# Kernel optimization log

Hardware: AMD Instinct MI355X
Metric: run time of the kernel (lower is better)

The kernel has to match this reference:

```python
import jax, jax.numpy as jnp
import numpy as np

UNITS, ORDER, THETA = 1024, 512, 784.0
T, B = 784, 128

def _lmu_AB(order, theta):
    # Legendre delay continuous-time state space, then ZOH discretization (dt=1)
    q = np.arange(order, dtype=np.float64)
    r = (2.0 * q + 1.0)[:, None] / theta
    i, j = np.meshgrid(q, q, indexing='ij')
    A = np.where(i < j, -1.0, (-1.0) ** (i - j + 1.0)) * r
    Bc = ((-1.0) ** q)[:, None] * r
    Ad = np.array(jax.scipy.linalg.expm(jnp.asarray(A, dtype=jnp.float32)), dtype=np.float64)
    Bd = np.linalg.solve(A, (Ad - np.eye(order)) @ Bc)
    # cell stores AT = Ad - I so that m <- m + m@AT^T + u@BT^T == m@Ad^T + u@Bd^T
    return (Ad - np.eye(order)).astype(np.float32), Bd.astype(np.float32)

def setup_inputs() -> dict:
    key = jax.random.key(0)
    ks = jax.random.split(key, 9)
    AT, BT = _lmu_AB(ORDER, THETA)
    xav = np.sqrt(2.0 / (UNITS + ORDER)).astype(np.float32)
    return {
        'inputs': jax.random.normal(ks[0], (T, B, 1), dtype=jnp.float32),
        'e_x': jax.random.normal(ks[1], (1, 1), dtype=jnp.float32),
        'e_h': jax.random.normal(ks[2], (1, UNITS), dtype=jnp.float32) * 0.02,
        'e_m': jax.random.normal(ks[3], (1, ORDER), dtype=jnp.float32) * 0.02,
        'W_x': jax.random.normal(ks[4], (UNITS, 1), dtype=jnp.float32) * 0.1,
        'W_h': jax.random.normal(ks[5], (UNITS, UNITS), dtype=jnp.float32) * 0.02,
        'W_m': jax.random.normal(ks[6], (UNITS, ORDER), dtype=jnp.float32) * xav,
        'AT': jnp.asarray(AT),
        'BT': jnp.asarray(BT),
        'W_dense': jax.random.normal(ks[7], (10, UNITS), dtype=jnp.float32) * 0.03,
        'b_dense': jax.random.normal(ks[8], (10,), dtype=jnp.float32) * 0.01,
    }

def reference(inputs, e_x, e_h, e_m, W_x, W_h, W_m, AT, BT, W_dense, b_dense):
    Bsz = inputs.shape[1]
    h0 = jnp.zeros((Bsz, W_h.shape[0]), inputs.dtype)
    m0 = jnp.zeros((Bsz, AT.shape[0]), inputs.dtype)
    def step(carry, x):  # x: (B, 1)
        h, m = carry
        u = x @ e_x.T + h @ e_h.T + m @ e_m.T            # (B, 1)
        m = m + m @ AT.T + u @ BT.T                       # linear Legendre memory update
        h = jnp.tanh(x @ W_x.T + h @ W_h.T + m @ W_m.T)  # nonlinear hidden update
        return (h, m), None
    (h, m), _ = jax.lax.scan(step, (h0, m0), inputs)
    logits = h @ W_dense.T + b_dense
    return jax.nn.softmax(logits, axis=-1)
```

## Files before the change

kernel.cpp:

```cpp
#include <hip/hip_runtime.h>
#include <hip/hip_fp16.h>
#include <cmath>


typedef _Float16 half8 __attribute__((ext_vector_type(8)));
typedef float floatx4 __attribute__((ext_vector_type(4)));

#define NSTATE   1536
#define BATCH    128
#define TSTEPS   784
#define KTILES   48
#define ISL_WGS  32
#define SLICE_H8 9216
#define LO_SCALE 2048.0f
#define LO_INV   (1.0f / 2048.0f)

__device__ __align__(16) _Float16 g_Whi[NSTATE * NSTATE];
__device__ __align__(16) _Float16 g_Wlo[NSTATE * NSTATE];
__device__ float    g_wb[NSTATE];
__device__ float    g_WmA[1024 * 512];
__device__ float    g_WmB[1024];
__device__ __align__(16) _Float16 g_Shi[2 * BATCH * NSTATE];
__device__ __align__(16) _Float16 g_Slo[2 * BATCH * NSTATE];
__device__ unsigned g_bar[1024];

__device__ __forceinline__ unsigned poll_rmw(unsigned* p) {
    unsigned old;
    asm volatile("global_atomic_add %0, %1, %2, off sc0\n\ts_waitcnt vmcnt(0)"
                 : "=&v"(old)
                 : "v"(p), "v"(0u)
                 : "memory");
    return old;
}

__device__ __forceinline__ float fast_tanh(float x) {
    float e = __expf(2.f * x);
    return 1.f - 2.f / (e + 1.f);
}

__global__ void prep_wmb(const float* __restrict__ Wm, const float* __restrict__ BT) {
    int row  = blockIdx.x * 4 + (threadIdx.x >> 6);
    int lane = threadIdx.x & 63;
    float s = 0.f;
    for (int c = lane; c < 512; c += 64) s += Wm[row * 512 + c] * BT[c];
    for (int o = 32; o; o >>= 1) s += __shfl_down(s, o);
    if (lane == 0) g_WmB[row] = s;
}

__global__ void prep_wma(const float* __restrict__ Wm, const float* __restrict__ AT) {
    __shared__ float As[32][33], Bs[32][33];
    int d0 = blockIdx.x * 32, i0 = blockIdx.y * 32;
    int tx = threadIdx.x & 31, ty = threadIdx.x >> 5;
    float acc[4];
#pragma unroll
    for (int r = 0; r < 4; ++r) acc[r] = Wm[(i0 + ty + 8 * r) * 512 + d0 + tx];
    for (int c0 = 0; c0 < 512; c0 += 32) {
#pragma unroll
        for (int r = 0; r < 4; ++r) {
            As[ty + 8 * r][tx] = Wm[(i0 + ty + 8 * r) * 512 + c0 + tx];
            Bs[ty + 8 * r][tx] = AT[(c0 + ty + 8 * r) * 512 + d0 + tx];
        }
        __syncthreads();
#pragma unroll
        for (int c = 0; c < 32; ++c)
#pragma unroll
            for (int r = 0; r < 4; ++r) acc[r] += As[ty + 8 * r][c] * Bs[c][tx];
        __syncthreads();
    }
#pragma unroll
    for (int r = 0; r < 4; ++r) g_WmA[(i0 + ty + 8 * r) * 512 + d0 + tx] = acc[r];
}

__global__ void prep_wfull(const float* __restrict__ Wh, const float* __restrict__ AT,
                           const float* __restrict__ BT, const float* __restrict__ eh,
                           const float* __restrict__ em, const float* __restrict__ ex,
                           const float* __restrict__ Wx) {
    int s = blockIdx.x * 256 + threadIdx.x;
    int j8 = s & 7;
    int u = s >> 3;
    int lane = u & 63;
    u >>= 6;
    int nt = u % 3; u /= 3;
    int kt = u % 48;
    int sl = u / 48;
    int n = sl * 48 + nt * 16 + (lane & 15);
    int k = kt * 32 + ((lane >> 4) & 3) * 8 + j8;

    float w;
    if (n < 1024) {
        if (k < 1024) w = Wh[n * 1024 + k] + g_WmB[n] * eh[k];
        else          w = g_WmA[n * 512 + (k - 1024)] + g_WmB[n] * em[k - 1024];
    } else {
        int c = n - 1024;
        if (k < 1024) w = BT[c] * eh[k];
        else {
            int d = k - 1024;
            w = ((c == d) ? 1.f : 0.f) + AT[c * 512 + d] + BT[c] * em[d];
        }
    }
    _Float16 hi = (_Float16)w;
    g_Whi[s] = hi;
    g_Wlo[s] = (_Float16)((w - (float)hi) * LO_SCALE);

    if (s < NSTATE) {
        float b = (s < 1024) ? (Wx[s] + ex[0] * g_WmB[s]) : (BT[s - 1024] * ex[0]);
        g_wb[s] = b;
    }
    if (s < 2 * BATCH * NSTATE) { g_Shi[s] = (_Float16)0.f; g_Slo[s] = (_Float16)0.f; }
    if (s < 1024) g_bar[s] = 0u;
}

__launch_bounds__(256, 1)
__global__ void lmu_persist(const float* __restrict__ inputs) {
    __shared__ half8  lwh[SLICE_H8];
    __shared__ float4 red[4 * 3 * 64];
    __shared__ int    s_sl;

    const int tid = threadIdx.x;

    unsigned xcd;
    asm volatile("s_getreg_b32 %0, hwreg(HW_REG_XCC_ID)" : "=s"(xcd));
    xcd &= 7u;
    if (tid == 0) {
        unsigned rank = __hip_atomic_fetch_add(g_bar + 512 + xcd * 64, 1u,
                                               __ATOMIC_RELAXED,
                                               __HIP_MEMORY_SCOPE_WORKGROUP);
        s_sl = (int)(rank & 31u);
    }
    __syncthreads();
    const int isl = (int)xcd;
    const int sl  = s_sl;

    {
        const half8* src = (const half8*)g_Whi + (size_t)sl * SLICE_H8;
        for (int i = tid; i < SLICE_H8; i += 256) lwh[i] = src[i];
    }

    const int lane = tid & 63, wv = tid >> 6;
    const int quad = lane >> 4, l16 = lane & 15;
    const int kt0 = wv * 12;
    const int rowA = isl * 16 + l16;
    unsigned* cnt = g_bar + isl * 64;

    const int ncol = sl * 48 + wv * 16 + l16;
    const float wbv = (wv < 3) ? g_wb[ncol] : 0.f;
    const bool do_tanh = (sl * 48 + wv * 16) < 1024;

    half8 wr[12 * 3];
    {
        const half8* wlo = (const half8*)g_Wlo + (size_t)sl * SLICE_H8;
#pragma unroll
        for (int ki = 0; ki < 12; ++ki)
#pragma unroll
            for (int nt = 0; nt < 3; ++nt)
                wr[ki * 3 + nt] = wlo[((kt0 + ki) * 3 + nt) * 64 + lane];
    }

    __syncthreads();

    int buf = 0;
    for (int t = 0; t < TSTEPS; ++t) {
        const _Float16* shr =
            g_Shi + buf * BATCH * NSTATE + rowA * NSTATE + quad * 8;
        const _Float16* slr =
            g_Slo + buf * BATCH * NSTATE + rowA * NSTATE + quad * 8;

        floatx4 aA[3], aB[3], aC[3];
#pragma unroll
        for (int q = 0; q < 3; ++q) { aA[q] = (floatx4)0.f; aB[q] = (floatx4)0.f; aC[q] = (floatx4)0.f; }

#pragma unroll
        for (int ki = 0; ki < 12; ++ki) {
            const int kt = kt0 + ki;
            half8 ah = *(const half8*)(shr + kt * 32);
            half8 al = *(const half8*)(slr + kt * 32);
#pragma unroll
            for (int nt = 0; nt < 3; ++nt) {
                half8 bh = lwh[(kt * 3 + nt) * 64 + lane];
                aA[nt] = __builtin_amdgcn_mfma_f32_16x16x32_f16(ah, bh, aA[nt], 0, 0, 0);
                aB[nt] = __builtin_amdgcn_mfma_f32_16x16x32_f16(al, bh, aB[nt], 0, 0, 0);
                aC[nt] = __builtin_amdgcn_mfma_f32_16x16x32_f16(ah, wr[ki * 3 + nt], aC[nt], 0, 0, 0);
            }
        }

#pragma unroll
        for (int nt = 0; nt < 3; ++nt) {
            floatx4 P = aA[nt] + (aB[nt] + aC[nt]) * LO_INV;
            red[(wv * 3 + nt) * 64 + lane] = float4{P[0], P[1], P[2], P[3]};
        }
        __syncthreads();

        const int nbuf = buf ^ 1;
        if (wv < 3) {
            float4 v0 = red[(0 * 3 + wv) * 64 + lane];
            float4 v1 = red[(1 * 3 + wv) * 64 + lane];
            float4 v2 = red[(2 * 3 + wv) * 64 + lane];
            float4 v3 = red[(3 * 3 + wv) * 64 + lane];
            float vr4[4] = {v0.x + v1.x + v2.x + v3.x, v0.y + v1.y + v2.y + v3.y,
                            v0.z + v1.z + v2.z + v3.z, v0.w + v1.w + v2.w + v3.w};
            _Float16* dh = g_Shi + nbuf * BATCH * NSTATE;
            _Float16* dl = g_Slo + nbuf * BATCH * NSTATE;
            const float* xt = inputs + t * BATCH + isl * 16 + quad * 4;
#pragma unroll
            for (int r = 0; r < 4; ++r) {
                int b = isl * 16 + quad * 4 + r;
                float v = vr4[r] + xt[r] * wbv;
                if (do_tanh) v = fast_tanh(v);
                _Float16 hi = (_Float16)v;
                dh[b * NSTATE + ncol] = hi;
                dl[b * NSTATE + ncol] = (_Float16)((v - (float)hi) * LO_SCALE);
            }
        }

        __builtin_amdgcn_fence(__ATOMIC_RELEASE, "workgroup");
        __syncthreads();
        if (tid == 0) {
            __hip_atomic_fetch_add(cnt, 1u, __ATOMIC_RELAXED,
                                   __HIP_MEMORY_SCOPE_WORKGROUP);
            const unsigned target = (unsigned)ISL_WGS * (unsigned)(t + 1);
            int spin = 0;
            while (poll_rmw(cnt) < target) {
                if (++spin > (1 << 18)) break;
            }
        }
        __syncthreads();
        asm volatile("buffer_inv\n\ts_waitcnt vmcnt(0)" ::: "memory");
        __builtin_amdgcn_fence(__ATOMIC_ACQUIRE, "workgroup");
        buf = nbuf;
    }
}

__global__ void lmu_out(const float* __restrict__ Wd, const float* __restrict__ bd,
                        float* __restrict__ out) {
    __shared__ float red[272];
    int b = blockIdx.x;
    const _Float16* sh = g_Shi + b * NSTATE;
    const _Float16* sl = g_Slo + b * NSTATE;
    int tid = threadIdx.x;
    int c = tid & 15, chunk = tid >> 4;
    float part = 0.f;
    if (c < 10) {
        for (int i = chunk * 64; i < chunk * 64 + 64; ++i)
            part += ((float)sh[i] + (float)sl[i] * LO_INV) * Wd[c * 1024 + i];
    }
    red[chunk * 16 + c] = part;
    __syncthreads();
    if (tid < 10) {
        float lg = bd[tid];
        for (int q = 0; q < 16; ++q) lg += red[q * 16 + tid];
        red[256 + tid] = lg;
    }
    __syncthreads();
    if (tid < 10) {
        float mx = red[256];
        for (int q = 1; q < 10; ++q) mx = fmaxf(mx, red[256 + q]);
        float sm = 0.f;
        for (int q = 0; q < 10; ++q) sm += expf(red[256 + q] - mx);
        out[b * 10 + tid] = expf(red[256 + tid] - mx) / sm;
    }
}

extern "C" void kernel_launch(void* const* d_in, const int* in_sizes, int n_in,
                              void* d_out, int out_size, void* d_ws, size_t ws_size,
                              hipStream_t stream) {
    const float* inputs = (const float*)d_in[0];
    const float* e_x    = (const float*)d_in[1];
    const float* e_h    = (const float*)d_in[2];
    const float* e_m    = (const float*)d_in[3];
    const float* W_x    = (const float*)d_in[4];
    const float* W_h    = (const float*)d_in[5];
    const float* W_m    = (const float*)d_in[6];
    const float* AT     = (const float*)d_in[7];
    const float* BT     = (const float*)d_in[8];
    const float* W_d    = (const float*)d_in[9];
    const float* b_d    = (const float*)d_in[10];
    (void)d_ws; (void)ws_size; (void)in_sizes; (void)n_in;

    prep_wmb<<<256, 256, 0, stream>>>(W_m, BT);
    prep_wma<<<dim3(16, 32), 256, 0, stream>>>(W_m, AT);
    prep_wfull<<<9216, 256, 0, stream>>>(W_h, AT, BT, e_h, e_m, e_x, W_x);

    lmu_persist<<<256, 256, 0, stream>>>(inputs);

    lmu_out<<<128, 256, 0, stream>>>(W_d, b_d, (float*)d_out);
}
```

Before: 3.910 ms.

## Split K across eight waves per workgroup with two-stage LDS reduction

The persistent LMU kernel goes from 4 to 8 waves per workgroup, and each wave covers 6 K-tiles instead of 12, so the per-wave MFMA chain and register-resident low-part weights are halved. Partial sums are reduced through LDS in two phases: waves 0-3 store, then waves 4-7 accumulate, with an extra barrier. The aim is to cut per-step latency on the serial recurrence by running more MFMA streams in parallel. The cost is one more __syncthreads per timestep and a launch bound of 2 blocks per CU, which may limit registers.

```diff
diff --git a/kernel.cpp b/kernel.cpp
--- a/kernel.cpp
+++ b/kernel.cpp
@@ -14,6 +14,8 @@
 #define SLICE_H8 9216
 #define LO_SCALE 2048.0f
 #define LO_INV   (1.0f / 2048.0f)
+#define NWAVES   8
+#define KI_W     6
 
 __device__ __align__(16) _Float16 g_Whi[NSTATE * NSTATE];
 __device__ __align__(16) _Float16 g_Wlo[NSTATE * NSTATE];
@@ -110,11 +112,11 @@
     if (s < 1024) g_bar[s] = 0u;
 }
 
-__launch_bounds__(256, 1)
+__launch_bounds__(512, 2)
 __global__ void lmu_persist(const float* __restrict__ inputs) {
-    __shared__ half8  lwh[SLICE_H8];
-    __shared__ float4 red[4 * 3 * 64];
-    __shared__ int    s_sl;
+    __shared__ half8   lwh[SLICE_H8];
+    __shared__ floatx4 red[4 * 3 * 64];
+    __shared__ int     s_sl;
 
     const int tid = threadIdx.x;
 
@@ -133,12 +135,12 @@
 
     {
         const half8* src = (const half8*)g_Whi + (size_t)sl * SLICE_H8;
-        for (int i = tid; i < SLICE_H8; i += 256) lwh[i] = src[i];
+        for (int i = tid; i < SLICE_H8; i += 512) lwh[i] = src[i];
     }
 
     const int lane = tid & 63, wv = tid >> 6;
     const int quad = lane >> 4, l16 = lane & 15;
-    const int kt0 = wv * 12;
+    const int kt0 = wv * KI_W;
     const int rowA = isl * 16 + l16;
     unsigned* cnt = g_bar + isl * 64;
 
@@ -146,11 +148,11 @@
     const float wbv = (wv < 3) ? g_wb[ncol] : 0.f;
     const bool do_tanh = (sl * 48 + wv * 16) < 1024;
 
-    half8 wr[12 * 3];
+    half8 wr[KI_W * 3];
     {
         const half8* wlo = (const half8*)g_Wlo + (size_t)sl * SLICE_H8;
 #pragma unroll
-        for (int ki = 0; ki < 12; ++ki)
+        for (int ki = 0; ki < KI_W; ++ki)
 #pragma unroll
             for (int nt = 0; nt < 3; ++nt)
                 wr[ki * 3 + nt] = wlo[((kt0 + ki) * 3 + nt) * 64 + lane];
@@ -170,7 +172,7 @@
         for (int q = 0; q < 3; ++q) { aA[q] = (floatx4)0.f; aB[q] = (floatx4)0.f; aC[q] = (floatx4)0.f; }
 
 #pragma unroll
-        for (int ki = 0; ki < 12; ++ki) {
+        for (int ki = 0; ki < KI_W; ++ki) {
             const int kt = kt0 + ki;
             half8 ah = *(const half8*)(shr + kt * 32);
             half8 al = *(const half8*)(slr + kt * 32);
@@ -183,28 +185,34 @@
             }
         }
 
-#pragma unroll
-        for (int nt = 0; nt < 3; ++nt) {
-            floatx4 P = aA[nt] + (aB[nt] + aC[nt]) * LO_INV;
-            red[(wv * 3 + nt) * 64 + lane] = float4{P[0], P[1], P[2], P[3]};
+        floatx4 P[3];
+#pragma unroll
+        for (int nt = 0; nt < 3; ++nt)
+            P[nt] = aA[nt] + (aB[nt] + aC[nt]) * LO_INV;
+        if (wv < 4) {
+#pragma unroll
+            for (int nt = 0; nt < 3; ++nt)
+                red[((wv & 3) * 3 + nt) * 64 + lane] = P[nt];
+        }
+        __syncthreads();
+        if (wv >= 4) {
+#pragma unroll
+            for (int nt = 0; nt < 3; ++nt)
+                red[((wv & 3) * 3 + nt) * 64 + lane] += P[nt];
         }
         __syncthreads();
 
         const int nbuf = buf ^ 1;
         if (wv < 3) {
-            float4 v0 = red[(0 * 3 + wv) * 64 + lane];
-            float4 v1 = red[(1 * 3 + wv) * 64 + lane];
-            float4 v2 = red[(2 * 3 + wv) * 64 + lane];
-            float4 v3 = red[(3 * 3 + wv) * 64 + lane];
-            float vr4[4] = {v0.x + v1.x + v2.x + v3.x, v0.y + v1.y + v2.y + v3.y,
-                            v0.z + v1.z + v2.z + v3.z, v0.w + v1.w + v2.w + v3.w};
+            floatx4 vs = red[(0 * 3 + wv) * 64 + lane] + red[(1 * 3 + wv) * 64 + lane]
+                       + red[(2 * 3 + wv) * 64 + lane] + red[(3 * 3 + wv) * 64 + lane];
             _Float16* dh = g_Shi + nbuf * BATCH * NSTATE;
             _Float16* dl = g_Slo + nbuf * BATCH * NSTATE;
             const float* xt = inputs + t * BATCH + isl * 16 + quad * 4;
 #pragma unroll
             for (int r = 0; r < 4; ++r) {
                 int b = isl * 16 + quad * 4 + r;
-                float v = vr4[r] + xt[r] * wbv;
+                float v = vs[r] + xt[r] * wbv;
                 if (do_tanh) v = fast_tanh(v);
                 _Float16 hi = (_Float16)v;
                 dh[b * NSTATE + ncol] = hi;
@@ -280,7 +288,7 @@
     prep_wma<<<dim3(16, 32), 256, 0, stream>>>(W_m, AT);
     prep_wfull<<<9216, 256, 0, stream>>>(W_h, AT, BT, e_h, e_m, e_x, W_x);
 
-    lmu_persist<<<256, 256, 0, stream>>>(inputs);
+    lmu_persist<<<256, 512, 0, stream>>>(inputs);
 
     lmu_out<<<128, 256, 0, stream>>>(W_d, b_d, (float*)d_out);
 }
```

Result: no change. 3.949 ms (+1.0%).
